# Optimization experiments

Hardware: AMD Instinct MI355X
Metric: run time of the kernel (lower is better)

## Reference

```python
import jax, jax.numpy as jnp
import numpy as np

BLOCK, HALO, HEADS = 8, 3, 4


def setup_inputs() -> dict:
    key = jax.random.key(0)
    k1, k2, k3, k4 = jax.random.split(key, 4)
    ch, d = 128, 128 // HEADS
    win = BLOCK + 2 * HALO
    return {
        "x": jax.random.normal(k1, (8, ch, 128, 128), dtype=jnp.float32),
        "qkv_w": jax.random.normal(k2, (3 * ch, ch), dtype=jnp.float32) * (2.0 / ch) ** 0.5,
        "rel_h": jax.random.normal(k3, (1, win, 1, d // 2), dtype=jnp.float32),
        "rel_w": jax.random.normal(k4, (1, 1, win, d // 2), dtype=jnp.float32),
    }


def _halo_windows(t, block, halo):
    b, c, h, w = t.shape
    win = block + 2 * halo
    nh, nw = h // block, w // block
    tp = jnp.pad(t, ((0, 0), (0, 0), (halo, halo), (halo, halo)))
    idx_h = (jnp.arange(nh) * block)[:, None] + jnp.arange(win)[None, :]
    idx_w = (jnp.arange(nw) * block)[:, None] + jnp.arange(win)[None, :]
    return tp[:, :, idx_h[:, None, :, None], idx_w[None, :, None, :]]


def reference(x, qkv_w, rel_h, rel_w):
    block, halo, heads = BLOCK, HALO, HEADS
    b, c, h, w = x.shape
    d = c // heads
    win = block + 2 * halo
    nh, nw = h // block, w // block

    # 1x1 conv (bias=False)
    qkv = jnp.einsum('bchw,oc->bohw', x, qkv_w)
    q, k, v = jnp.split(qkv, 3, axis=1)

    # q: non-overlapping blocks -> (b, nh, nw, heads, block*block, d), scaled
    q = q.reshape(b, heads, d, nh, block, nw, block)
    q = q.transpose(0, 3, 5, 1, 4, 6, 2).reshape(b, nh, nw, heads, block * block, d)
    q = q * d ** -0.5

    kw = _halo_windows(k, block, halo)
    vw = _halo_windows(v, block, halo)
    kw = kw.reshape(b, heads, d, nh, nw, win, win).transpose(0, 3, 4, 1, 5, 6, 2)
    vw = vw.reshape(b, heads, d, nh, nw, win, win).transpose(0, 3, 4, 1, 5, 6, 2)
    vw = vw.reshape(b, nh, nw, heads, win * win, d)

    # relative position bias added to keys (first half varies over rows, second over cols)
    k_h, k_w2 = jnp.split(kw, 2, axis=-1)
    kw = jnp.concatenate([k_h + rel_h, k_w2 + rel_w], axis=-1)
    kw = kw.reshape(b, nh, nw, heads, win * win, d)

    sim = jnp.einsum('...id,...jd->...ij', q, kw)
    attn = jax.nn.softmax(sim, axis=-1)
    out = jnp.einsum('...ij,...jd->...id', attn, vw)  # (b,nh,nw,heads, blk^2, d)

    # reassemble: channel = (head, d) head-major; rows = (nh, k1); cols = (nw, k2)
    out = out.reshape(b, nh, nw, heads, block, block, d)
    out = out.transpose(0, 3, 6, 1, 4, 2, 5).reshape(b, c, h, w)
    return out
```

## Files before the change

### kernel.cpp

```cpp
#include <hip/hip_runtime.h>
#include <hip/hip_bf16.h>


typedef __attribute__((ext_vector_type(8))) short bf16x8;
typedef __attribute__((ext_vector_type(4))) short bf16x4;
typedef __attribute__((ext_vector_type(4))) float f32x4;
union BF8 { bf16x8 v; unsigned u[4]; };
union BF4 { bf16x4 v; unsigned u[2]; };

#define DEVI static __device__ __forceinline__

DEVI short f2bf(float f) {
    __bf16 h = (__bf16)f;
    union { __bf16 h; short s; } c; c.h = h; return c.s;
}
DEVI unsigned pk2(float a, float b) {
    return (unsigned)(unsigned short)f2bf(a) | ((unsigned)(unsigned short)f2bf(b) << 16);
}

#if defined(__has_builtin)
#  if __has_builtin(__builtin_amdgcn_mfma_f32_16x16x16bf16_1k)
#    define HAVE_MFMA16_1K 1
#  endif
#endif

DEVI f32x4 mfma16(bf16x4 a, bf16x4 b, f32x4 c) {
#ifdef HAVE_MFMA16_1K
    return __builtin_amdgcn_mfma_f32_16x16x16bf16_1k(a, b, c, 0, 0, 0);
#else
    f32x4 d;
    asm("v_mfma_f32_16x16x16_bf16 %0, %1, %2, %3" : "=v"(d) : "v"(a), "v"(b), "v"(c));
    return d;
#endif
}

#define QSCALE (0.17677669529663687f * 1.4426950408889634f)

__global__ void wcvt(const float* __restrict__ w, short* __restrict__ ws_w) {
    int e = blockIdx.x * 256 + threadIdx.x;
    if (e < 384 * 128) {
        float v = w[e];
        if (e < 128 * 128) v *= QSCALE;
        ws_w[e] = f2bf(v);
    }
}

__launch_bounds__(256)
__global__ void qkv_gemm(const float* __restrict__ x, const short* __restrict__ ws_w,
                         short* __restrict__ ws_q, short* __restrict__ ws_k,
                         short* __restrict__ ws_v) {
    const int blk = blockIdx.x;
    const int b = blk >> 6;
    const int pixbase = (blk & 63) << 8;
    const int tid = threadIdx.x, wv = tid >> 6, ln = tid & 63;
    const int lr = ln & 15, lg = ln >> 4;
    const int n0 = pixbase + wv * 64;
    const f32x4 zz = {0.f, 0.f, 0.f, 0.f};

    BF8 Bx[4][4];
    #pragma unroll
    for (int nt = 0; nt < 4; ++nt) {
        const int pix = n0 + nt * 16 + lr;
        #pragma unroll
        for (int ks = 0; ks < 4; ++ks) {
            const float* xp = x + (((size_t)((b << 7) + ks * 32 + lg * 8)) << 14) + pix;
            float f[8];
            #pragma unroll
            for (int e = 0; e < 8; ++e) f[e] = xp[(size_t)e << 14];
            Bx[nt][ks].u[0] = pk2(f[0], f[1]); Bx[nt][ks].u[1] = pk2(f[2], f[3]);
            Bx[nt][ks].u[2] = pk2(f[4], f[5]); Bx[nt][ks].u[3] = pk2(f[6], f[7]);
        }
    }

    for (int ot = 0; ot < 24; ++ot) {
        bf16x8 Aw[4];
        #pragma unroll
        for (int ks = 0; ks < 4; ++ks)
            Aw[ks] = *(const bf16x8*)&ws_w[(ot * 16 + lr) * 128 + ks * 32 + lg * 8];
        f32x4 acc[4];
        #pragma unroll
        for (int nt = 0; nt < 4; ++nt) {
            acc[nt] = zz;
            #pragma unroll
            for (int ks = 0; ks < 4; ++ks)
                acc[nt] = __builtin_amdgcn_mfma_f32_16x16x32_bf16(Aw[ks], Bx[nt][ks].v, acc[nt], 0, 0, 0);
        }
        if (ot < 8) {
            const int head = ot >> 1, dd0 = ((ot & 1) << 4) + lg * 4;
            #pragma unroll
            for (int nt = 0; nt < 4; ++nt) {
                const int pix = n0 + nt * 16 + lr;
                const int gr = pix >> 7, gc = pix & 127;
                const int ii = gr >> 3, jj = gc >> 3;
                const int qrow = ((gr & 7) << 3) | (gc & 7);
                size_t off = ((size_t)((((b * 16 + ii) * 16 + jj) << 2) + head) << 11) + qrow * 32 + dd0;
                *(uint2*)&ws_q[off] = make_uint2(pk2(acc[nt][0], acc[nt][1]), pk2(acc[nt][2], acc[nt][3]));
            }
        } else if (ot < 16) {
            const int head = (ot - 8) >> 1, dd0 = (((ot - 8) & 1) << 4) + lg * 4;
            const size_t kb = ((size_t)(b * 4 + head)) << 19;
            #pragma unroll
            for (int nt = 0; nt < 4; ++nt) {
                const int pix = n0 + nt * 16 + lr;
                *(uint2*)&ws_k[kb + pix * 32 + dd0] =
                    make_uint2(pk2(acc[nt][0], acc[nt][1]), pk2(acc[nt][2], acc[nt][3]));
            }
        } else {
            const int vch = ((ot - 16) << 4) + lg * 4;
            const int head = vch >> 5, dd = vch & 31;
            #pragma unroll
            for (int nt = 0; nt < 4; ++nt) {
                const int pix = n0 + nt * 16 + lr;
                const int gr = pix >> 7, gc = pix & 127;
                const size_t base = ((((size_t)(b * 4 + head) << 7) + gr) * 32 + dd) * 136 + 3 + gc;
                #pragma unroll
                for (int r = 0; r < 4; ++r) ws_v[base + r * 136] = f2bf(acc[nt][r]);
            }
        }
    }
}

template<bool EDGE>
DEVI void attn_body(int b, int i, int j, int head, int ln, int mt0,
                    const short* __restrict__ ws_q, const short* __restrict__ ws_k,
                    const short* __restrict__ ws_v,
                    const float* __restrict__ rel_h, const float* __restrict__ rel_w,
                    float* __restrict__ out) {
    const int lr = ln & 15, lg = ln >> 4;
    const f32x4 zz = {0.f, 0.f, 0.f, 0.f};
    const int bh = b * 4 + head;

    const short* qbase = ws_q + ((size_t)((((b * 16 + i) * 16 + j) << 2) + head) << 11);
    const short* kbase = ws_k + (((size_t)bh) << 19);
    const short* vbase = ws_v + (size_t)bh * (128 * 32 * 136);

    bf16x8 Bq[2];
    #pragma unroll
    for (int m = 0; m < 2; ++m)
        Bq[m] = *(const bf16x8*)&qbase[((mt0 + m) * 16 + lr) * 32 + lg * 8];

    BF8 Ah, Awf;
    #pragma unroll
    for (int wd = 0; wd < 4; ++wd) { Ah.u[wd] = 0u; Awf.u[wd] = 0u; }
    if (lr < 14) {
        if (lg < 2) {
            const float* rp = rel_h + lr * 16 + lg * 8;
            #pragma unroll
            for (int wd = 0; wd < 4; ++wd) Ah.u[wd] = pk2(rp[2 * wd], rp[2 * wd + 1]);
        } else {
            const float* rp = rel_w + lr * 16 + (lg - 2) * 8;
            #pragma unroll
            for (int wd = 0; wd < 4; ++wd) Awf.u[wd] = pk2(rp[2 * wd], rp[2 * wd + 1]);
        }
    }
    f32x4 qh4[2], qw4[2];
    #pragma unroll
    for (int m = 0; m < 2; ++m) {
        qh4[m] = __builtin_amdgcn_mfma_f32_16x16x32_bf16(Ah.v, Bq[m], zz, 0, 0, 0);
        qw4[m] = __builtin_amdgcn_mfma_f32_16x16x32_bf16(Awf.v, Bq[m], zz, 0, 0, 0);
    }
    if (lg == 3) {
        #pragma unroll
        for (int m = 0; m < 2; ++m) { qw4[m][2] = -16384.f; qw4[m][3] = -16384.f; }
    }

    BF4 Bones; Bones.u[0] = 0x3F803F80u; Bones.u[1] = 0x3F803F80u;

    const int gc   = j * 8 - 3 + lr;
    const int gcc  = EDGE ? min(max(gc, 0), 127) : gc;
    const bool gcBad = EDGE && (gc != gcc);
    const int colb = j * 8 + lg * 4;
    unsigned mmc0 = 0xFFFFFFFFu, mmc1 = 0xFFFFFFFFu;
    if (EDGE) {
        const int gc0 = colb - 3;
        const int lo = max(0, -gc0), hi = min(3, 127 - gc0);
        const unsigned bits = (lo <= hi) ? (((0xFu >> (3 - (hi - lo))) << lo) & 0xFu) : 0u;
        mmc0 = ((bits & 1u) ? 0x0000FFFFu : 0u) | ((bits & 2u) ? 0xFFFF0000u : 0u);
        mmc1 = ((bits & 4u) ? 0x0000FFFFu : 0u) | ((bits & 8u) ? 0xFFFF0000u : 0u);
    }

    f32x4 a0[2] = {zz, zz}, a1[2] = {zz, zz}, sA[2] = {zz, zz};
    #pragma unroll
    for (int t = 0; t < 14; ++t) {
        const int gr = i * 8 - 3 + t;
        const bool grOK = !EDGE || ((unsigned)gr < 128u);
        const int grc = EDGE ? min(max(gr, 0), 127) : gr;

        BF8 Ak;
        Ak.v = *(const bf16x8*)&kbase[((grc << 7) + gcc) * 32 + lg * 8];
        if (EDGE && (gcBad || !grOK)) { Ak.u[0] = 0; Ak.u[1] = 0; Ak.u[2] = 0; Ak.u[3] = 0; }

        BF4 Bv0, Bv1;
        *(uint2*)Bv0.u = *(const uint2*)&vbase[((grc << 5) + lr) * 136 + colb];
        *(uint2*)Bv1.u = *(const uint2*)&vbase[((grc << 5) + 16 + lr) * 136 + colb];
        if (EDGE) {
            const unsigned mm0 = grOK ? mmc0 : 0u;
            const unsigned mm1 = grOK ? mmc1 : 0u;
            Bv0.u[0] &= mm0; Bv0.u[1] &= mm1; Bv1.u[0] &= mm0; Bv1.u[1] &= mm1;
        }

        #pragma unroll
        for (int m = 0; m < 2; ++m) {
            const float qh = __shfl(qh4[m][t & 3], ((t >> 2) << 4) | lr, 64);
            f32x4 cin;
            #pragma unroll
            for (int r = 0; r < 4; ++r) cin[r] = qw4[m][r] + qh;
            const f32x4 p = __builtin_amdgcn_mfma_f32_16x16x32_bf16(Ak.v, Bq[m], cin, 0, 0, 0);
            BF4 Ap;
            Ap.u[0] = pk2(exp2f(p[0]), exp2f(p[1]));
            Ap.u[1] = pk2(exp2f(p[2]), exp2f(p[3]));
            a0[m] = mfma16(Ap.v, Bv0.v, a0[m]);
            a1[m] = mfma16(Ap.v, Bv1.v, a1[m]);
            sA[m] = mfma16(Ap.v, Bones.v, sA[m]);
        }
    }

    #pragma unroll
    for (int m = 0; m < 2; ++m) {
        f32x4 acc0, acc1;
        #pragma unroll
        for (int r = 0; r < 4; ++r) {
            const float rinv = __builtin_amdgcn_rcpf(sA[m][r]);
            acc0[r] = a0[m][r] * rinv;
            acc1[r] = a1[m][r] * rinv;
        }
        const int qb = (mt0 + m) * 16 + lg * 4;
        float* op = out + (((size_t)(b * 128 + head * 32)) << 14)
                        + ((i * 8 + (qb >> 3)) << 7) + j * 8 + (qb & 7);
        *(f32x4*)(op + ((size_t)lr << 14)) = acc0;
        *(f32x4*)(op + ((size_t)(16 + lr) << 14)) = acc1;
    }
}

__launch_bounds__(256)
__global__ void attn4(const short* __restrict__ ws_q, const short* __restrict__ ws_k,
                      const short* __restrict__ ws_v,
                      const float* __restrict__ rel_h, const float* __restrict__ rel_w,
                      float* __restrict__ out) {
    const int bid = blockIdx.x;
    const int blk = ((bid & 7) << 9) | (bid >> 3);
    const int half = blk & 1, j = (blk >> 1) & 15, i = (blk >> 5) & 15, b = blk >> 9;
    const int head = threadIdx.x >> 6, ln = threadIdx.x & 63;
    if (i == 0 || i == 15 || j == 0 || j == 15)
        attn_body<true>(b, i, j, head, ln, half * 2, ws_q, ws_k, ws_v, rel_h, rel_w, out);
    else
        attn_body<false>(b, i, j, head, ln, half * 2, ws_q, ws_k, ws_v, rel_h, rel_w, out);
}

__launch_bounds__(256, 2)
__global__ void halo_attn(const float* __restrict__ x,
                          const float* __restrict__ qkv_w,
                          const float* __restrict__ relh_g,
                          const float* __restrict__ relw_g,
                          float* __restrict__ out)
{
    const int blk  = blockIdx.x;
    const int head = blk & 3;
    const int j    = (blk >> 2) & 15;
    const int i    = (blk >> 6) & 15;
    const int b    = blk >> 10;
    const int tid = threadIdx.x;
    const int wv  = tid >> 6;
    const int ln  = tid & 63;
    const int lr  = ln & 15;
    const int lg  = ln >> 4;

    __shared__ __align__(16) union { short xs[112*128]; short pbuf[64*224]; } XP;
    __shared__ __align__(16) short kbuf[208*32];
    __shared__ __align__(16) short vbufT[32*224];
    __shared__ __align__(16) short qbuf[64*32];
    __shared__ float smax[4*64];
    __shared__ float ssum[4*64];
    __shared__ float relh[224];
    __shared__ float relw[224];

    for (int t = tid; t < 32*224/2; t += 256) ((int*)vbufT)[t] = 0;
    for (int t = tid; t < 224; t += 256) { relh[t] = relh_g[t]; relw[t] = relw_g[t]; }

    bf16x8 Bw[6][4];
    #pragma unroll
    for (int n = 0; n < 6; ++n) {
        const int obase = (n < 2) ? head*32 + n*16
                        : (n < 4) ? 128 + head*32 + (n-2)*16
                                  : 256 + head*32 + (n-4)*16;
        const float* wp0 = qkv_w + (obase + lr)*128;
        #pragma unroll
        for (int ks = 0; ks < 4; ++ks) {
            const float* wp = wp0 + ks*32 + lg*8;
            bf16x8 f;
            #pragma unroll
            for (int e = 0; e < 8; ++e) f[e] = f2bf(wp[e]);
            Bw[n][ks] = f;
        }
    }

    for (int ph = 0; ph < 2; ++ph) {
        __syncthreads();
        for (int t = tid; t < 112*128; t += 256) {
            const int ch = t / 112;
            const int p  = t - ch*112;
            float val = 0.f;
            if (p < 98) {
                const int P  = ph*98 + p;
                const int wr = P / 14, wc = P - wr*14;
                const int gr = i*8 - 3 + wr, gc = j*8 - 3 + wc;
                if ((unsigned)gr < 128u && (unsigned)gc < 128u)
                    val = x[((b*128 + ch)*128 + gr)*128 + gc];
            }
            XP.xs[p*128 + (ch & 7) + 8*((ch >> 3) ^ (p & 15))] = f2bf(val);
        }
        __syncthreads();

        for (int mt = wv; mt < 7; mt += 4) {
            const int row = mt*16 + lr;
            bf16x8 A[4];
            #pragma unroll
            for (int ks = 0; ks < 4; ++ks)
                A[ks] = *(const bf16x8*)&XP.xs[row*128 + 8*((ks*4 + lg) ^ (row & 15))];
            #pragma unroll
            for (int n = 0; n < 6; ++n) {
                f32x4 acc = {0.f, 0.f, 0.f, 0.f};
                #pragma unroll
                for (int ks = 0; ks < 4; ++ks)
                    acc = __builtin_amdgcn_mfma_f32_16x16x32_bf16(A[ks], Bw[n][ks], acc, 0, 0, 0);
                #pragma unroll
                for (int r = 0; r < 4; ++r) {
                    const int p = mt*16 + lg*4 + r;
                    if (p >= 98) continue;
                    const int P  = ph*98 + p;
                    const int wr = P / 14, wc = P - wr*14;
                    const float val = acc[r];
                    if (n < 2) {
                        if (wr >= 3 && wr <= 10 && wc >= 3 && wc <= 10) {
                            const int qi = (wr-3)*8 + (wc-3);
                            const int dd = n*16 + lr;
                            qbuf[qi*32 + (dd & 7) + 8*((dd >> 3) ^ ((qi >> 1) & 3))] =
                                f2bf(val * 0.17677669529663687f);
                        }
                    } else if (n < 4) {
                        const int dd = (n-2)*16 + lr;
                        const float bias = (dd < 16) ? relh[wr*16 + dd] : relw[wc*16 + dd - 16];
                        kbuf[P*32 + (dd & 7) + 8*((dd >> 3) ^ ((P >> 1) & 3))] = f2bf(val + bias);
                    } else {
                        const int dd = (n-4)*16 + lr;
                        vbufT[dd*224 + (P & 7) + 8*((P >> 3) ^ ((dd >> 1) & 3))] = f2bf(val);
                    }
                }
            }
        }
    }
    __syncthreads();

    bf16x8 Aq[4];
    #pragma unroll
    for (int mt = 0; mt < 4; ++mt) {
        const int row = mt*16 + lr;
        Aq[mt] = *(const bf16x8*)&qbuf[row*32 + 8*(lg ^ ((row >> 1) & 3))];
    }

    f32x4 sim[4][4];
    #pragma unroll
    for (int ntl = 0; ntl < 4; ++ntl) {
        const int nt = wv + ntl*4;
        if (nt > 12) continue;
        const int P = nt*16 + lr;
        const bf16x8 Bk = *(const bf16x8*)&kbuf[P*32 + 8*(lg ^ ((P >> 1) & 3))];
        #pragma unroll
        for (int mt = 0; mt < 4; ++mt) {
            const f32x4 z = {0.f, 0.f, 0.f, 0.f};
            sim[ntl][mt] = __builtin_amdgcn_mfma_f32_16x16x32_bf16(Aq[mt], Bk, z, 0, 0, 0);
        }
    }

    for (int t = tid; t < 64*224/2; t += 256) ((int*)XP.pbuf)[t] = 0;

    #pragma unroll
    for (int mt = 0; mt < 4; ++mt)
    #pragma unroll
    for (int r = 0; r < 4; ++r) {
        float m = -1e30f;
        #pragma unroll
        for (int ntl = 0; ntl < 4; ++ntl) {
            const int nt = wv + ntl*4;
            if (nt > 12) continue;
            const int key = nt*16 + lr;
            if (key < 196) m = fmaxf(m, sim[ntl][mt][r]);
        }
        #pragma unroll
        for (int off = 1; off < 16; off <<= 1)
            m = fmaxf(m, __shfl_xor(m, off, 64));
        if (lr == 0) smax[wv*64 + mt*16 + lg*4 + r] = m;
    }
    __syncthreads();

    #pragma unroll
    for (int mt = 0; mt < 4; ++mt)
    #pragma unroll
    for (int r = 0; r < 4; ++r) {
        const int qrow = mt*16 + lg*4 + r;
        const float gm = fmaxf(fmaxf(smax[qrow], smax[64+qrow]),
                               fmaxf(smax[128+qrow], smax[192+qrow]));
        float s = 0.f;
        #pragma unroll
        for (int ntl = 0; ntl < 4; ++ntl) {
            const int nt = wv + ntl*4;
            if (nt > 12) continue;
            const int key = nt*16 + lr;
            float e = (key < 196) ? __expf(sim[ntl][mt][r] - gm) : 0.f;
            sim[ntl][mt][r] = e;
            s += e;
        }
        #pragma unroll
        for (int off = 1; off < 16; off <<= 1)
            s += __shfl_xor(s, off, 64);
        if (lr == 0) ssum[wv*64 + qrow] = s;
    }
    __syncthreads();

    #pragma unroll
    for (int mt = 0; mt < 4; ++mt)
    #pragma unroll
    for (int r = 0; r < 4; ++r) {
        const int qrow = mt*16 + lg*4 + r;
        const float rinv = 1.f / (ssum[qrow] + ssum[64+qrow] + ssum[128+qrow] + ssum[192+qrow]);
        #pragma unroll
        for (int ntl = 0; ntl < 4; ++ntl) {
            const int nt = wv + ntl*4;
            if (nt > 12) continue;
            const int key = nt*16 + lr;
            XP.pbuf[qrow*224 + (key & 7) + 8*((key >> 3) ^ ((qrow >> 1) & 3))] =
                f2bf(sim[ntl][mt][r] * rinv);
        }
    }
    __syncthreads();

    f32x4 oacc[2] = {{0.f,0.f,0.f,0.f},{0.f,0.f,0.f,0.f}};
    const int mt = wv;
    #pragma unroll
    for (int ks = 0; ks < 7; ++ks) {
        const int row = mt*16 + lr;
        const int g = ks*4 + lg;
        const bf16x8 Ap = *(const bf16x8*)&XP.pbuf[row*224 + 8*(g ^ ((row >> 1) & 3))];
        #pragma unroll
        for (int n = 0; n < 2; ++n) {
            const int dd = n*16 + lr;
            const bf16x8 Bv = *(const bf16x8*)&vbufT[dd*224 + 8*(g ^ ((dd >> 1) & 3))];
            oacc[n] = __builtin_amdgcn_mfma_f32_16x16x32_bf16(Ap, Bv, oacc[n], 0, 0, 0);
        }
    }

    #pragma unroll
    for (int n = 0; n < 2; ++n) {
        const int dd = n*16 + lr;
        const int c  = head*32 + dd;
        const int qb = mt*16 + lg*4;
        const int rb = qb >> 3, cb = qb & 7;
        float* op = out + ((b*128 + c)*128 + (i*8 + rb))*128 + j*8 + cb;
        *(f32x4*)op = oacc[n];
    }
}

extern "C" void kernel_launch(void* const* d_in, const int* in_sizes, int n_in,
                              void* d_out, int out_size, void* d_ws, size_t ws_size,
                              hipStream_t stream)
{
    const float* x  = (const float*)d_in[0];
    const float* w  = (const float*)d_in[1];
    const float* rh = (const float*)d_in[2];
    const float* rw = (const float*)d_in[3];
    float* o = (float*)d_out;

    const size_t Q_ELEMS = (size_t)8192 * 2048;
    const size_t K_ELEMS = (size_t)32 * 16384 * 32;
    const size_t V_ELEMS = (size_t)32 * 128 * 32 * 136;
    const size_t W_ELEMS = (size_t)384 * 128;
    const size_t NEED = (Q_ELEMS + K_ELEMS + V_ELEMS + W_ELEMS) * 2 + 1024;

    if (ws_size >= NEED) {
        short* ws_q = (short*)d_ws;
        short* ws_k = ws_q + Q_ELEMS;
        short* ws_v = ws_k + K_ELEMS;
        short* ws_w = ws_v + V_ELEMS;
        wcvt<<<dim3(192), dim3(256), 0, stream>>>(w, ws_w);
        qkv_gemm<<<dim3(512), dim3(256), 0, stream>>>(x, ws_w, ws_q, ws_k, ws_v);
        attn4<<<dim3(4096), dim3(256), 0, stream>>>(ws_q, ws_k, ws_v, rh, rw, o);
    } else {
        halo_attn<<<dim3(8192), dim3(256), 0, stream>>>(x, w, rh, rw, o);
    }
}
```

Baseline: 114.5 us.

## Store V unpadded via transposed MFMA, preload K rows, use raw v_exp

The QKV GEMM now computes the V tile with swapped MFMA operands, so each lane holds four consecutive pixels. It writes them as packed 8-byte stores into an unpadded 128-wide V layout, replacing the scattered 2-byte stores into a 136-wide padded layout. The attention body reads V from the unpadded rows with two unaligned-window loads realigned by alignbit, and relies on the existing edge masks instead of zero padding. It also preloads all 14 K rows into registers before the loop and replaces exp2f with an inline v_exp_f32. These changes raise register pressure and read slightly outside row bounds, where the values are masked off.

```diff
diff --git a/kernel.cpp b/kernel.cpp
--- a/kernel.cpp
+++ b/kernel.cpp
@@ -16,6 +16,9 @@
 }
 DEVI unsigned pk2(float a, float b) {
     return (unsigned)(unsigned short)f2bf(a) | ((unsigned)(unsigned short)f2bf(b) << 16);
+}
+DEVI float fexp2(float x) {
+    float r; asm("v_exp_f32 %0, %1\n\ts_nop 0" : "=v"(r) : "v"(x)); return r;
 }
 
 #if defined(__has_builtin)
@@ -77,44 +80,55 @@
         #pragma unroll
         for (int ks = 0; ks < 4; ++ks)
             Aw[ks] = *(const bf16x8*)&ws_w[(ot * 16 + lr) * 128 + ks * 32 + lg * 8];
-        f32x4 acc[4];
-        #pragma unroll
-        for (int nt = 0; nt < 4; ++nt) {
-            acc[nt] = zz;
-            #pragma unroll
-            for (int ks = 0; ks < 4; ++ks)
-                acc[nt] = __builtin_amdgcn_mfma_f32_16x16x32_bf16(Aw[ks], Bx[nt][ks].v, acc[nt], 0, 0, 0);
-        }
-        if (ot < 8) {
-            const int head = ot >> 1, dd0 = ((ot & 1) << 4) + lg * 4;
+
+        if (ot < 16) {
+            f32x4 acc[4];
             #pragma unroll
             for (int nt = 0; nt < 4; ++nt) {
-                const int pix = n0 + nt * 16 + lr;
-                const int gr = pix >> 7, gc = pix & 127;
-                const int ii = gr >> 3, jj = gc >> 3;
-                const int qrow = ((gr & 7) << 3) | (gc & 7);
-                size_t off = ((size_t)((((b * 16 + ii) * 16 + jj) << 2) + head) << 11) + qrow * 32 + dd0;
-                *(uint2*)&ws_q[off] = make_uint2(pk2(acc[nt][0], acc[nt][1]), pk2(acc[nt][2], acc[nt][3]));
+                acc[nt] = zz;
+                #pragma unroll
+                for (int ks = 0; ks < 4; ++ks)
+                    acc[nt] = __builtin_amdgcn_mfma_f32_16x16x32_bf16(Aw[ks], Bx[nt][ks].v, acc[nt], 0, 0, 0);
             }
-        } else if (ot < 16) {
-            const int head = (ot - 8) >> 1, dd0 = (((ot - 8) & 1) << 4) + lg * 4;
-            const size_t kb = ((size_t)(b * 4 + head)) << 19;
-            #pragma unroll
-            for (int nt = 0; nt < 4; ++nt) {
-                const int pix = n0 + nt * 16 + lr;
-                *(uint2*)&ws_k[kb + pix * 32 + dd0] =
-                    make_uint2(pk2(acc[nt][0], acc[nt][1]), pk2(acc[nt][2], acc[nt][3]));
+            if (ot < 8) {
+                const int head = ot >> 1, dd0 = ((ot & 1) << 4) + lg * 4;
+                #pragma unroll
+                for (int nt = 0; nt < 4; ++nt) {
+                    const int pix = n0 + nt * 16 + lr;
+                    const int gr = pix >> 7, gc = pix & 127;
+                    const int ii = gr >> 3, jj = gc >> 3;
+                    const int qrow = ((gr & 7) << 3) | (gc & 7);
+                    size_t off = ((size_t)((((b * 16 + ii) * 16 + jj) << 2) + head) << 11) + qrow * 32 + dd0;
+                    *(uint2*)&ws_q[off] = make_uint2(pk2(acc[nt][0], acc[nt][1]), pk2(acc[nt][2], acc[nt][3]));
+                }
+            } else {
+                const int head = (ot - 8) >> 1, dd0 = (((ot - 8) & 1) << 4) + lg * 4;
+                const size_t kb = ((size_t)(b * 4 + head)) << 19;
+                #pragma unroll
+                for (int nt = 0; nt < 4; ++nt) {
+                    const int pix = n0 + nt * 16 + lr;
+                    *(uint2*)&ws_k[kb + pix * 32 + dd0] =
+                        make_uint2(pk2(acc[nt][0], acc[nt][1]), pk2(acc[nt][2], acc[nt][3]));
+                }
             }
         } else {
-            const int vch = ((ot - 16) << 4) + lg * 4;
-            const int head = vch >> 5, dd = vch & 31;
+            const int vch = ((ot - 16) << 4) + lr;
+            const int headv = vch >> 5, dv = vch & 31;
+            f32x4 accT[4];
             #pragma unroll
             for (int nt = 0; nt < 4; ++nt) {
-                const int pix = n0 + nt * 16 + lr;
-                const int gr = pix >> 7, gc = pix & 127;
-                const size_t base = ((((size_t)(b * 4 + head) << 7) + gr) * 32 + dd) * 136 + 3 + gc;
+                accT[nt] = zz;
                 #pragma unroll
-                for (int r = 0; r < 4; ++r) ws_v[base + r * 136] = f2bf(acc[nt][r]);
+                for (int ks = 0; ks < 4; ++ks)
+                    accT[nt] = __builtin_amdgcn_mfma_f32_16x16x32_bf16(Bx[nt][ks].v, Aw[ks], accT[nt], 0, 0, 0);
+            }
+            #pragma unroll
+            for (int nt = 0; nt < 4; ++nt) {
+                const int pixq = n0 + nt * 16 + lg * 4;
+                const int gr = pixq >> 7, gcq = pixq & 127;
+                const size_t idx = ((((size_t)(b * 4 + headv) * 128 + gr) * 32 + dv) << 7) + gcq;
+                *(uint2*)&ws_v[idx] =
+                    make_uint2(pk2(accT[nt][0], accT[nt][1]), pk2(accT[nt][2], accT[nt][3]));
             }
         }
     }
@@ -132,7 +146,7 @@
 
     const short* qbase = ws_q + ((size_t)((((b * 16 + i) * 16 + j) << 2) + head) << 11);
     const short* kbase = ws_k + (((size_t)bh) << 19);
-    const short* vbase = ws_v + (size_t)bh * (128 * 32 * 136);
+    const short* vbase = ws_v + (size_t)bh * (128 * 32 * 128);
 
     bf16x8 Bq[2];
     #pragma unroll
@@ -169,14 +183,24 @@
     const int gc   = j * 8 - 3 + lr;
     const int gcc  = EDGE ? min(max(gc, 0), 127) : gc;
     const bool gcBad = EDGE && (gc != gcc);
-    const int colb = j * 8 + lg * 4;
+    const int w0   = j * 8 - 3 + lg * 4;
     unsigned mmc0 = 0xFFFFFFFFu, mmc1 = 0xFFFFFFFFu;
     if (EDGE) {
-        const int gc0 = colb - 3;
-        const int lo = max(0, -gc0), hi = min(3, 127 - gc0);
+        const int lo = max(0, -w0), hi = min(3, 127 - w0);
         const unsigned bits = (lo <= hi) ? (((0xFu >> (3 - (hi - lo))) << lo) & 0xFu) : 0u;
         mmc0 = ((bits & 1u) ? 0x0000FFFFu : 0u) | ((bits & 2u) ? 0xFFFF0000u : 0u);
         mmc1 = ((bits & 4u) ? 0x0000FFFFu : 0u) | ((bits & 8u) ? 0xFFFF0000u : 0u);
+    }
+
+    BF8 Ak[14];
+    #pragma unroll
+    for (int t = 0; t < 14; ++t) {
+        const int gr = i * 8 - 3 + t;
+        const int grc = EDGE ? min(max(gr, 0), 127) : gr;
+        Ak[t].v = *(const bf16x8*)&kbase[((grc << 7) + gcc) * 32 + lg * 8];
+        if (EDGE && (gcBad || (unsigned)gr >= 128u)) {
+            Ak[t].u[0] = 0; Ak[t].u[1] = 0; Ak[t].u[2] = 0; Ak[t].u[3] = 0;
+        }
     }
 
     f32x4 a0[2] = {zz, zz}, a1[2] = {zz, zz}, sA[2] = {zz, zz};
@@ -186,13 +210,17 @@
         const bool grOK = !EDGE || ((unsigned)gr < 128u);
         const int grc = EDGE ? min(max(gr, 0), 127) : gr;
 
-        BF8 Ak;
-        Ak.v = *(const bf16x8*)&kbase[((grc << 7) + gcc) * 32 + lg * 8];
-        if (EDGE && (gcBad || !grOK)) { Ak.u[0] = 0; Ak.u[1] = 0; Ak.u[2] = 0; Ak.u[3] = 0; }
-
+        const short* vr0 = vbase + ((size_t)(grc * 32 + lr) << 7);
+        const uint2 lo0 = *(const uint2*)&vr0[w0 - 1];
+        const unsigned hi0 = *(const unsigned*)&vr0[w0 + 3];
+        const short* vr1 = vr0 + (16 << 7);
+        const uint2 lo1 = *(const uint2*)&vr1[w0 - 1];
+        const unsigned hi1 = *(const unsigned*)&vr1[w0 + 3];
         BF4 Bv0, Bv1;
-        *(uint2*)Bv0.u = *(const uint2*)&vbase[((grc << 5) + lr) * 136 + colb];
-        *(uint2*)Bv1.u = *(const uint2*)&vbase[((grc << 5) + 16 + lr) * 136 + colb];
+        Bv0.u[0] = __builtin_amdgcn_alignbit(lo0.y, lo0.x, 16);
+        Bv0.u[1] = __builtin_amdgcn_alignbit(hi0, lo0.y, 16);
+        Bv1.u[0] = __builtin_amdgcn_alignbit(lo1.y, lo1.x, 16);
+        Bv1.u[1] = __builtin_amdgcn_alignbit(hi1, lo1.y, 16);
         if (EDGE) {
             const unsigned mm0 = grOK ? mmc0 : 0u;
             const unsigned mm1 = grOK ? mmc1 : 0u;
@@ -205,10 +233,10 @@
             f32x4 cin;
             #pragma unroll
             for (int r = 0; r < 4; ++r) cin[r] = qw4[m][r] + qh;
-            const f32x4 p = __builtin_amdgcn_mfma_f32_16x16x32_bf16(Ak.v, Bq[m], cin, 0, 0, 0);
+            const f32x4 p = __builtin_amdgcn_mfma_f32_16x16x32_bf16(Ak[t].v, Bq[m], cin, 0, 0, 0);
             BF4 Ap;
-            Ap.u[0] = pk2(exp2f(p[0]), exp2f(p[1]));
-            Ap.u[1] = pk2(exp2f(p[2]), exp2f(p[3]));
+            Ap.u[0] = pk2(fexp2(p[0]), fexp2(p[1]));
+            Ap.u[1] = pk2(fexp2(p[2]), fexp2(p[3]));
             a0[m] = mfma16(Ap.v, Bv0.v, a0[m]);
             a1[m] = mfma16(Ap.v, Bv1.v, a1[m]);
             sA[m] = mfma16(Ap.v, Bones.v, sA[m]);
@@ -472,7 +500,7 @@
 
     const size_t Q_ELEMS = (size_t)8192 * 2048;
     const size_t K_ELEMS = (size_t)32 * 16384 * 32;
-    const size_t V_ELEMS = (size_t)32 * 128 * 32 * 136;
+    const size_t V_ELEMS = (size_t)32 * 128 * 32 * 128;
     const size_t W_ELEMS = (size_t)384 * 128;
     const size_t NEED = (Q_ELEMS + K_ELEMS + V_ELEMS + W_ELEMS) * 2 + 1024;
 
```

New measurement: 166.3 us. 45.2% more time.
